# Performance work log

Measured on AMD Instinct MI355X. Metric: run time of the kernel, lower is better.

Reference implementation:

```python
import jax, jax.numpy as jnp
import numpy as np

N_LAYERS = 2
H = 16                      # num_heads
ARW = (1.0, 1.0)            # att_residual_weight
MCB = (0.0, 1.0)            # mask_clip_balancer
LN_EPS = 1e-5


def _ln(x, g, b):
    mu = jnp.mean(x, axis=-1, keepdims=True)
    var = jnp.mean(jnp.square(x - mu), axis=-1, keepdims=True)
    return (x - mu) * jax.lax.rsqrt(var + LN_EPS) * g + b


def _quick_gelu(u):
    return u * jax.nn.sigmoid(1.702 * u)


def setup_inputs() -> dict:
    key = jax.random.key(0)
    ks = jax.random.split(key, 8)
    L, B, C = 577, 8, 1024
    d_ff = 4 * C
    inp = {
        'x': jax.random.normal(ks[0], (L, B, C), jnp.float32),
        'att_bias': jax.random.normal(ks[1], (N_LAYERS, B * H, L, L), jnp.float32),
        'ln1_g': jnp.ones((N_LAYERS, C), jnp.float32),
        'ln1_b': jnp.zeros((N_LAYERS, C), jnp.float32),
        'in_w': 0.02 * jax.random.normal(ks[2], (N_LAYERS, 3 * C, C), jnp.float32),
        'in_b': jnp.zeros((N_LAYERS, 3 * C), jnp.float32),
        'out_w': 0.02 * jax.random.normal(ks[3], (N_LAYERS, C, C), jnp.float32),
        'out_b': jnp.zeros((N_LAYERS, C), jnp.float32),
        'ln2_g': jnp.ones((N_LAYERS, C), jnp.float32),
        'ln2_b': jnp.zeros((N_LAYERS, C), jnp.float32),
        'fc1_w': 0.02 * jax.random.normal(ks[4], (N_LAYERS, d_ff, C), jnp.float32),
        'fc1_b': jnp.zeros((N_LAYERS, d_ff), jnp.float32),
        'fc2_w': 0.02 * jax.random.normal(ks[5], (N_LAYERS, C, d_ff), jnp.float32),
        'fc2_b': jnp.zeros((N_LAYERS, C), jnp.float32),
    }
    return inp


def reference(x, att_bias, ln1_g, ln1_b, in_w, in_b, out_w, out_b,
              ln2_g, ln2_b, fc1_w, fc1_b, fc2_w, fc2_b):
    L, B, C = x.shape
    d = C // H
    scale = d ** -0.5  # custom_att_factor is None
    for i in range(N_LAYERS):
        # --- custom CSA attention ---
        h = _ln(x, ln1_g[i], ln1_b[i])                              # [L,B,C]
        qkv = jnp.einsum('lbc,fc->lbf', h, in_w[i]) + in_b[i]       # [L,B,3C]
        q, k, v = jnp.split(qkv, 3, axis=-1)
        to_heads = lambda t: t.reshape(L, B, H, d).transpose(1, 2, 0, 3)  # [B,H,L,d]
        q, k, v = to_heads(q), to_heads(k), to_heads(v)
        bias = att_bias[i].reshape(B, H, L, L)
        q_attn = bias + scale * jnp.einsum('bhld,bhmd->bhlm', q, q)
        k_attn = bias + scale * jnp.einsum('bhld,bhmd->bhlm', k, k)
        attn = jax.nn.softmax(q_attn, axis=-1) + jax.nn.softmax(k_attn, axis=-1)
        attn = attn * 0.5                                           # norm_att=True
        attn = jnp.mean(attn, axis=1, keepdims=True)                # avg_att=True -> [B,1,L,L]
        out = jnp.matmul(attn, v)                                   # broadcast over H -> [B,H,L,d]
        out = MCB[0] * v + MCB[1] * out
        out = out.transpose(2, 0, 1, 3).reshape(L, B, C)
        out = jnp.einsum('lbc,oc->lbo', out, out_w[i]) + out_b[i]
        x = ARW[0] * x + ARW[1] * out
        # --- MLP residual ---
        h2 = _ln(x, ln2_g[i], ln2_b[i])
        u = _quick_gelu(jnp.einsum('lbc,fc->lbf', h2, fc1_w[i]) + fc1_b[i])
        x = x + jnp.einsum('lbf,cf->lbc', u, fc2_w[i]) + fc2_b[i]
    return x
```

## Files before the change

kernel.cpp:

```cpp
#include <hip/hip_runtime.h>

typedef float f32x4 __attribute__((ext_vector_type(4)));
typedef __bf16 bf16x8 __attribute__((ext_vector_type(8)));

#define L_SEQ 577
#define BB 8
#define CC 1024
#define HH 16
#define ROWS (L_SEQ*BB)

static __device__ __forceinline__ ushort f2b(float f) {
  unsigned u = __float_as_uint(f);
  u += 0x7fffu + ((u >> 16) & 1u);
  return (ushort)(u >> 16);
}

static __device__ __forceinline__ void gld16(const void* g, void* l) {
  __builtin_amdgcn_global_load_lds((const __attribute__((address_space(1))) void*)g,
                                   (__attribute__((address_space(3))) void*)l, 16, 0, 0);
}

__global__ void cvt4_kernel(const float* __restrict__ s0, ushort* __restrict__ d0, int n0,
                            const float* __restrict__ s1, ushort* __restrict__ d1, int n1,
                            const float* __restrict__ s2, ushort* __restrict__ d2, int n2,
                            const float* __restrict__ s3, ushort* __restrict__ d3, int n3)
{
  int i = blockIdx.x * blockDim.x + threadIdx.x;
  const float* src; ushort* dst;
  if (i < n0)                { src = s0; dst = d0; }
  else if ((i -= n0) < n1)   { src = s1; dst = d1; }
  else if ((i -= n1) < n2)   { src = s2; dst = d2; }
  else if ((i -= n2) < n3)   { src = s3; dst = d3; }
  else return;
  float4 v = *(const float4*)(src + (size_t)i * 4);
  ushort4 o;
  o.x = f2b(v.x); o.y = f2b(v.y); o.z = f2b(v.z); o.w = f2b(v.w);
  *(ushort4*)(dst + (size_t)i * 4) = o;
}

template<int NP, bool DOLN>
__global__ __launch_bounds__(256)
void ln_resid_kernel(const float* __restrict__ xsrc, const float* __restrict__ parts,
                     const float* __restrict__ cbias,
                     const float* __restrict__ g, const float* __restrict__ be,
                     float* __restrict__ xdst, ushort* __restrict__ hout)
{
  const int row = blockIdx.x;
  const int t = threadIdx.x;
  float4 v = *(const float4*)(xsrc + (size_t)row * CC + t * 4);
  if (NP > 0) {
    float4 c4 = *(const float4*)(cbias + t * 4);
    v.x += c4.x; v.y += c4.y; v.z += c4.z; v.w += c4.w;
    #pragma unroll
    for (int p = 0; p < NP; ++p) {
      float4 pv = *(const float4*)(parts + ((size_t)p * ROWS + row) * CC + t * 4);
      v.x += pv.x; v.y += pv.y; v.z += pv.z; v.w += pv.w;
    }
  }
  *(float4*)(xdst + (size_t)row * CC + t * 4) = v;
  if (DOLN) {
    float s  = v.x + v.y + v.z + v.w;
    float s2 = v.x*v.x + v.y*v.y + v.z*v.z + v.w*v.w;
    #pragma unroll
    for (int sd = 1; sd < 64; sd <<= 1) { s += __shfl_xor(s, sd, 64); s2 += __shfl_xor(s2, sd, 64); }
    __shared__ float ps[4], ps2[4];
    const int w = t >> 6;
    if ((t & 63) == 0) { ps[w] = s; ps2[w] = s2; }
    __syncthreads();
    s  = ps[0] + ps[1] + ps[2] + ps[3];
    s2 = ps2[0] + ps2[1] + ps2[2] + ps2[3];
    const float mean = s * (1.f / 1024.f);
    const float var  = s2 * (1.f / 1024.f) - mean * mean;
    const float rstd = rsqrtf(var + 1e-5f);
    float4 gv = *(const float4*)(g + t * 4);
    float4 bv = *(const float4*)(be + t * 4);
    ushort4 o;
    o.x = f2b((v.x - mean) * rstd * gv.x + bv.x);
    o.y = f2b((v.y - mean) * rstd * gv.y + bv.y);
    o.z = f2b((v.z - mean) * rstd * gv.z + bv.z);
    o.w = f2b((v.w - mean) * rstd * gv.w + bv.w);
    *(ushort4*)(hout + (size_t)row * CC + t * 4) = o;
  }
}

__global__ __launch_bounds__(256)
void vt_kernel(const ushort* __restrict__ qkv, ushort* __restrict__ vt)
{
  __shared__ ushort tile[32][33];
  const int lt = blockIdx.x * 32;
  const int nt = blockIdx.y * 32;
  const int b  = blockIdx.z;
  const int tx = threadIdx.x & 31;
  const int ty = threadIdx.x >> 5;
  #pragma unroll
  for (int p = 0; p < 4; ++p) {
    int l = lt + ty + p * 8;
    ushort v = 0;
    if (l < L_SEQ) v = qkv[((size_t)l * BB + b) * 3072 + 2048 + nt + tx];
    tile[ty + p * 8][tx] = v;
  }
  __syncthreads();
  #pragma unroll
  for (int p = 0; p < 4; ++p) {
    int n = nt + ty + p * 8;
    int l = lt + tx;
    vt[((size_t)b * 1024 + n) * 608 + l] = tile[tx][ty + p * 8];
  }
}

__global__ __launch_bounds__(512, 4)
void attn_kernel(const ushort* __restrict__ qkv,
                 const float* __restrict__ bias,
                 ushort* __restrict__ attnp)
{
  __shared__ float2 red[2][2][8][16];
  const int t = threadIdx.x;
  const int lane = t & 63;
  const int w = t >> 6;
  const int fr = lane & 15;
  const int lq = lane >> 4;
  const int id = blockIdx.x;
  const int b  = id & 7;
  const int rem = id >> 3;
  const int rb = rem % 37;
  const int hg = rem / 37;
  const int r0 = rb * 16;
  const int rowl = min(r0 + fr, L_SEQ - 1);
  const size_t rbase = ((size_t)rowl * BB + b) * 3072;
  const int kc = lq * 8;

  float acc[5][4];
  #pragma unroll
  for (int it = 0; it < 5; ++it)
    #pragma unroll
    for (int r = 0; r < 4; ++r) acc[it][r] = 0.f;

  for (int h4 = 0; h4 < 4; ++h4) {
    const int h = hg * 4 + h4;
    const int qoff = h * 64;
    const int koff = CC + h * 64;
    const bf16x8 rfq0 = *(const bf16x8*)(qkv + rbase + qoff + kc);
    const bf16x8 rfq1 = *(const bf16x8*)(qkv + rbase + qoff + 32 + kc);
    const bf16x8 rfk0 = *(const bf16x8*)(qkv + rbase + koff + kc);
    const bf16x8 rfk1 = *(const bf16x8*)(qkv + rbase + koff + 32 + kc);
    const float* brow = bias + (((size_t)(b * HH + h)) * L_SEQ + rowl) * L_SEQ;
    float sq[5][4], sk[5][4];
    #pragma unroll
    for (int it = 0; it < 5; ++it) {
      const int nt = w + it * 8;
      if (nt < 37) {
        const int crow = min(nt * 16 + fr, L_SEQ - 1);
        const size_t cb = ((size_t)crow * BB + b) * 3072;
        const bf16x8 bq0 = *(const bf16x8*)(qkv + cb + qoff + kc);
        const bf16x8 bq1 = *(const bf16x8*)(qkv + cb + qoff + 32 + kc);
        const bf16x8 bk0 = *(const bf16x8*)(qkv + cb + koff + kc);
        const bf16x8 bk1 = *(const bf16x8*)(qkv + cb + koff + 32 + kc);
        const int c0 = nt * 16 + lq * 4;
        float bs[4];
        #pragma unroll
        for (int r = 0; r < 4; ++r) bs[r] = brow[min(c0 + r, L_SEQ - 1)];
        f32x4 dq = {0.f, 0.f, 0.f, 0.f};
        f32x4 dk = {0.f, 0.f, 0.f, 0.f};
        dq = __builtin_amdgcn_mfma_f32_16x16x32_bf16(bq0, rfq0, dq, 0, 0, 0);
        dq = __builtin_amdgcn_mfma_f32_16x16x32_bf16(bq1, rfq1, dq, 0, 0, 0);
        dk = __builtin_amdgcn_mfma_f32_16x16x32_bf16(bk0, rfk0, dk, 0, 0, 0);
        dk = __builtin_amdgcn_mfma_f32_16x16x32_bf16(bk1, rfk1, dk, 0, 0, 0);
        #pragma unroll
        for (int r = 0; r < 4; ++r) {
          const bool cv = (c0 + r < L_SEQ);
          sq[it][r] = cv ? (bs[r] + 0.125f * dq[r]) : -1e30f;
          sk[it][r] = cv ? (bs[r] + 0.125f * dk[r]) : -1e30f;
        }
      } else {
        #pragma unroll
        for (int r = 0; r < 4; ++r) { sq[it][r] = -1e30f; sk[it][r] = -1e30f; }
      }
    }
    float mwq = -1e30f, mwk = -1e30f;
    #pragma unroll
    for (int it = 0; it < 5; ++it)
      #pragma unroll
      for (int r = 0; r < 4; ++r) { mwq = fmaxf(mwq, sq[it][r]); mwk = fmaxf(mwk, sk[it][r]); }
    mwq = fmaxf(mwq, __shfl_xor(mwq, 16, 64)); mwq = fmaxf(mwq, __shfl_xor(mwq, 32, 64));
    mwk = fmaxf(mwk, __shfl_xor(mwk, 16, 64)); mwk = fmaxf(mwk, __shfl_xor(mwk, 32, 64));
    float swq = 0.f, swk = 0.f;
    #pragma unroll
    for (int it = 0; it < 5; ++it)
      #pragma unroll
      for (int r = 0; r < 4; ++r) {
        sq[it][r] = __expf(sq[it][r] - mwq); swq += sq[it][r];
        sk[it][r] = __expf(sk[it][r] - mwk); swk += sk[it][r];
      }
    swq += __shfl_xor(swq, 16, 64); swq += __shfl_xor(swq, 32, 64);
    swk += __shfl_xor(swk, 16, 64); swk += __shfl_xor(swk, 32, 64);
    const int p = h4 & 1;
    if (lane < 16) {
      red[p][0][w][lane] = make_float2(mwq, swq);
      red[p][1][w][lane] = make_float2(mwk, swk);
    }
    __syncthreads();
    float mq = -1e30f, mk = -1e30f;
    #pragma unroll
    for (int ww = 0; ww < 8; ++ww) {
      mq = fmaxf(mq, red[p][0][ww][fr].x);
      mk = fmaxf(mk, red[p][1][ww][fr].x);
    }
    float smq = 0.f, smk = 0.f;
    #pragma unroll
    for (int ww = 0; ww < 8; ++ww) {
      const float2 pq = red[p][0][ww][fr];
      const float2 pk = red[p][1][ww][fr];
      smq += pq.y * __expf(pq.x - mq);
      smk += pk.y * __expf(pk.x - mk);
    }
    const float fq = 0.03125f * __expf(mwq - mq) / smq;
    const float fk = 0.03125f * __expf(mwk - mk) / smk;
    #pragma unroll
    for (int it = 0; it < 5; ++it)
      #pragma unroll
      for (int r = 0; r < 4; ++r) acc[it][r] += sq[it][r] * fq + sk[it][r] * fk;
  }
  if (r0 + fr < L_SEQ) {
    ushort* dst = attnp + ((size_t)hg * 8 + b) * 608 * 608 + (size_t)(r0 + fr) * 608;
    #pragma unroll
    for (int it = 0; it < 5; ++it) {
      const int nt = w + it * 8;
      if (nt < 37) {
        ushort4 o;
        o.x = f2b(acc[it][0]); o.y = f2b(acc[it][1]);
        o.z = f2b(acc[it][2]); o.w = f2b(acc[it][3]);
        *(ushort4*)(dst + nt * 16 + lq * 4) = o;
      }
    }
  }
}

__global__ __launch_bounds__(256)
void attn_combine(const ushort* __restrict__ attnp, ushort* __restrict__ attn)
{
  const int t = threadIdx.x;
  if (t >= 152) return;
  const int l = blockIdx.x;
  const int b = blockIdx.y;
  const int c0 = t * 4;
  const size_t base = ((size_t)b * 608 + l) * 608 + c0;
  const size_t hs = (size_t)8 * 608 * 608;
  float s[4] = {0.f, 0.f, 0.f, 0.f};
  #pragma unroll
  for (int p = 0; p < 4; ++p) {
    ushort4 v = *(const ushort4*)(attnp + p * hs + base);
    s[0] += __uint_as_float((unsigned)v.x << 16);
    s[1] += __uint_as_float((unsigned)v.y << 16);
    s[2] += __uint_as_float((unsigned)v.z << 16);
    s[3] += __uint_as_float((unsigned)v.w << 16);
  }
  ushort4 o;
  const bool lv = (l < L_SEQ);
  o.x = (lv && c0 + 0 < L_SEQ) ? f2b(s[0]) : (ushort)0;
  o.y = (lv && c0 + 1 < L_SEQ) ? f2b(s[1]) : (ushort)0;
  o.z = (lv && c0 + 2 < L_SEQ) ? f2b(s[2]) : (ushort)0;
  o.w = (lv && c0 + 3 < L_SEQ) ? f2b(s[3]) : (ushort)0;
  *(ushort4*)(attn + base) = o;
}

__global__ __launch_bounds__(256, 2)
void av_gemm(const ushort* __restrict__ A, int lda, int Arows, long aStride,
             const ushort* __restrict__ B, int ldb, long bStride,
             int M, int K,
             ushort* __restrict__ outb, int ldo)
{
  __shared__ __align__(16) ushort As[128 * 32];
  __shared__ __align__(16) ushort Bs[128 * 32];
  const int t = threadIdx.x;
  const int lane = t & 63;
  const int w = t >> 6;
  const int bm = blockIdx.x, bn = blockIdx.y, bz = blockIdx.z;
  const ushort* Ab = A + (long)bz * aStride;
  const ushort* Bb = B + (long)bz * bStride;
  const int srow = t >> 2;
  const int sc = (t & 3) * 8;
  const int wr = (w >> 1) * 64;
  const int wc = (w & 1) * 64;
  const int am1 = Arows - 1;
  f32x4 acc[4][4] = {};

  const int r0a = bm * 128 + srow;
  const int r0b = bn * 128 + srow;
  for (int kt = 0; kt < K; kt += 32) {
    __syncthreads();
    gld16(Ab + (size_t)min(r0a, am1) * lda + kt + sc, (void*)(As + t * 8));
    gld16(Ab + (size_t)min(r0a + 64, am1) * lda + kt + sc, (void*)(As + 2048 + t * 8));
    gld16(Bb + (size_t)r0b * ldb + kt + sc, (void*)(Bs + t * 8));
    gld16(Bb + (size_t)(r0b + 64) * ldb + kt + sc, (void*)(Bs + 2048 + t * 8));
    asm volatile("s_waitcnt vmcnt(0)" ::: "memory");
    __syncthreads();
    bf16x8 av[4], bv[4];
    const int fr = lane & 15;
    const int kc = (lane >> 4) * 8;
    #pragma unroll
    for (int m = 0; m < 4; ++m) av[m] = *(const bf16x8*)(As + (wr + m * 16 + fr) * 32 + kc);
    #pragma unroll
    for (int n = 0; n < 4; ++n) bv[n] = *(const bf16x8*)(Bs + (wc + n * 16 + fr) * 32 + kc);
    #pragma unroll
    for (int m = 0; m < 4; ++m)
      #pragma unroll
      for (int n = 0; n < 4; ++n)
        acc[m][n] = __builtin_amdgcn_mfma_f32_16x16x32_bf16(av[m], bv[n], acc[m][n], 0, 0, 0);
  }
  const int rbase = wr + (lane >> 4) * 4;
  const int cbase = wc + (lane & 15);
  #pragma unroll
  for (int n = 0; n < 4; ++n) {
    const int gn = bn * 128 + cbase + n * 16;
    #pragma unroll
    for (int m = 0; m < 4; ++m) {
      f32x4 d = acc[m][n];
      #pragma unroll
      for (int r = 0; r < 4; ++r) {
        const int gm = bm * 128 + rbase + m * 16 + r;
        if (gm < M) outb[((size_t)gm * 8 + bz) * ldo + gn] = f2b(d[r]);
      }
    }
  }
}

#define RD_A8(BOFS, MH) \
  _Pragma("unroll") for (int ks = 0; ks < 2; ++ks) \
  _Pragma("unroll") for (int m = 0; m < 4; ++m) \
    Af[ks][m] = rdA(BOFS, MH, ks, m);

#define RD_B4(BOFS, NH) \
  _Pragma("unroll") for (int ks = 0; ks < 2; ++ks) \
  _Pragma("unroll") for (int n = 0; n < 2; ++n) \
    Bf[NH][ks][n] = rdB(BOFS, NH, ks, n);

#define MFQ(MH, NH) \
  _Pragma("unroll") for (int ks = 0; ks < 2; ++ks) \
  _Pragma("unroll") for (int m = 0; m < 4; ++m) \
  _Pragma("unroll") for (int n = 0; n < 2; ++n) \
    acc[(MH)*4+m][(NH)*2+n] = __builtin_amdgcn_mfma_f32_16x16x32_bf16( \
        Af[ks][m], Bf[NH][ks][n], acc[(MH)*4+m][(NH)*2+n], 0, 0, 0);

#define BARO() \
  __builtin_amdgcn_sched_barrier(0); \
  __builtin_amdgcn_s_barrier(); \
  asm volatile("s_waitcnt lgkmcnt(0)" ::: "memory"); \
  __builtin_amdgcn_sched_barrier(0); \
  __builtin_amdgcn_s_setprio(1);

#define MF_END() \
  __builtin_amdgcn_s_setprio(0); \
  __builtin_amdgcn_sched_barrier(0); \
  __builtin_amdgcn_s_barrier();

template<int EPI>
__global__ __launch_bounds__(512, 2)
void gemm8(const ushort* __restrict__ Ap, int lda, int Arows,
           const ushort* __restrict__ Bp, int ldb,
           int M, int Ksplit,
           const float* __restrict__ bias,
           ushort* __restrict__ outb, float* __restrict__ outf, int ldo)
{
  __shared__ __align__(16) char smem[131072];
  const int t = threadIdx.x;
  const int lane = t & 63;
  const int w = t >> 6;
  const int wm = w >> 2, wn = w & 3;
  const int gx = gridDim.x;
  const int nwg = gx * gridDim.y;
  int id = blockIdx.y * gx + blockIdx.x;
  {
    const int q8 = nwg >> 3, r8 = nwg & 7;
    const int xcd = id & 7, pos = id >> 3;
    id = (xcd < r8 ? xcd * (q8 + 1) : r8 * (q8 + 1) + (xcd - r8) * q8) + pos;
  }
  const int bm = id % gx, bn = id / gx;
  const int bz = blockIdx.z;
  const int k0 = bz * Ksplit;
  const int iters = Ksplit >> 7;
  const int fr = lane & 15, lq = lane >> 4;

  f32x4 acc[8][4] = {};
  bf16x8 Af[2][4];
  bf16x8 Bf[2][2][2];

  const int rowj0 = t >> 3,        cbj0 = t & 7;
  const int rowj1 = (t + 512) >> 3, cbj1 = (t + 512) & 7;
  const ushort* pA[2][2]; const ushort* pB[2][2];
  #pragma unroll
  for (int h = 0; h < 2; ++h) {
    pA[h][0] = Ap + (size_t)min(bm*256 + h*128 + rowj0, Arows-1) * lda + k0 + ((cbj0 ^ (rowj0 & 7)) << 3);
    pA[h][1] = Ap + (size_t)min(bm*256 + h*128 + rowj1, Arows-1) * lda + k0 + ((cbj1 ^ (rowj1 & 7)) << 3);
    pB[h][0] = Bp + (size_t)(bn*256 + h*128 + rowj0) * ldb + k0 + ((cbj0 ^ (rowj0 & 7)) << 3);
    pB[h][1] = Bp + (size_t)(bn*256 + h*128 + rowj1) * ldb + k0 + ((cbj1 ^ (rowj1 & 7)) << 3);
  }

  auto stA = [&](int kt, int bofs, int h) {
    gld16(pA[h][0] + kt * 64, smem + bofs + h * 16384 + t * 16);
    gld16(pA[h][1] + kt * 64, smem + bofs + h * 16384 + (t + 512) * 16);
  };
  auto stB = [&](int kt, int bofs, int h) {
    gld16(pB[h][0] + kt * 64, smem + bofs + 32768 + h * 16384 + t * 16);
    gld16(pB[h][1] + kt * 64, smem + bofs + 32768 + h * 16384 + (t + 512) * 16);
  };
  auto rdA = [&](int bofs, int mh, int ks, int m) -> bf16x8 {
    const int rl = wm * 64 + m * 16 + fr;
    const int cb = (ks * 4 + lq) ^ (fr & 7);
    return *(const bf16x8*)(smem + bofs + mh * 16384 + rl * 128 + cb * 16);
  };
  auto rdB = [&](int bofs, int nh, int ks, int n) -> bf16x8 {
    const int rl = wn * 32 + n * 16 + fr;
    const int cb = (ks * 4 + lq) ^ (fr & 7);
    return *(const bf16x8*)(smem + bofs + 32768 + nh * 16384 + rl * 128 + cb * 16);
  };

  stA(0, 0, 0); stB(0, 0, 0); stB(0, 0, 1); stA(0, 0, 1);
  stA(1, 65536, 0); stB(1, 65536, 1); stA(1, 65536, 1);
  asm volatile("s_waitcnt vmcnt(6)" ::: "memory");
  __builtin_amdgcn_sched_barrier(0);
  __builtin_amdgcn_s_barrier();

  for (int i = 0; i < iters; ++i) {
    const bool more = (i + 1 < iters);
    const int kt2 = 2 * i + 2;
    RD_A8(0, 0) RD_B4(0, 0)
    stB(2 * i + 1, 65536, 0);
    BARO(); MFQ(0, 0) MF_END();
    RD_B4(0, 1)
    if (more) stA(kt2, 0, 0);
    BARO(); MFQ(0, 1) MF_END();
    RD_A8(0, 1)
    if (more) stB(kt2, 0, 1);
    BARO(); MFQ(1, 1) MF_END();
    if (more) stA(kt2, 0, 1);
    BARO(); MFQ(1, 0)
    __builtin_amdgcn_s_setprio(0);
    if (more) { asm volatile("s_waitcnt vmcnt(6)" ::: "memory"); }
    else      { asm volatile("s_waitcnt vmcnt(0)" ::: "memory"); }
    __builtin_amdgcn_sched_barrier(0);
    __builtin_amdgcn_s_barrier();
    RD_A8(65536, 0) RD_B4(65536, 0)
    if (more) stB(kt2, 0, 0);
    BARO(); MFQ(0, 0) MF_END();
    RD_B4(65536, 1)
    if (more) stA(2 * i + 3, 65536, 0);
    BARO(); MFQ(0, 1) MF_END();
    RD_A8(65536, 1)
    if (more) stB(2 * i + 3, 65536, 1);
    BARO(); MFQ(1, 1) MF_END();
    if (more) stA(2 * i + 3, 65536, 1);
    BARO(); MFQ(1, 0)
    __builtin_amdgcn_s_setprio(0);
    if (more) { asm volatile("s_waitcnt vmcnt(6)" ::: "memory"); }
    __builtin_amdgcn_sched_barrier(0);
    __builtin_amdgcn_s_barrier();
  }

  #pragma unroll
  for (int mh = 0; mh < 2; ++mh)
  #pragma unroll
  for (int nh = 0; nh < 2; ++nh)
  #pragma unroll
  for (int n = 0; n < 2; ++n) {
    const int gn = bn * 256 + nh * 128 + wn * 32 + n * 16 + fr;
    const float bval = (EPI == 4) ? 0.f : bias[gn];
    #pragma unroll
    for (int m = 0; m < 4; ++m) {
      f32x4 d = acc[mh * 4 + m][nh * 2 + n];
      #pragma unroll
      for (int r = 0; r < 4; ++r) {
        const int gm = bm * 256 + mh * 128 + wm * 64 + m * 16 + lq * 4 + r;
        if (gm < M) {
          if (EPI == 0) {
            outb[(size_t)gm * ldo + gn] = f2b(d[r] + bval);
          } else if (EPI == 1) {
            float v0 = d[r] + bval;
            outb[(size_t)gm * ldo + gn] = f2b(v0 / (1.f + __expf(-1.702f * v0)));
          } else {
            outf[((size_t)bz * M + gm) * ldo + gn] = d[r];
          }
        }
      }
    }
  }
}

extern "C" void kernel_launch(void* const* d_in, const int* in_sizes, int n_in,
                              void* d_out, int out_size, void* d_ws, size_t ws_size,
                              hipStream_t stream)
{
  (void)in_sizes; (void)n_in; (void)out_size; (void)ws_size;
  const float* x_in  = (const float*)d_in[0];
  const float* attb  = (const float*)d_in[1];
  const float* ln1_g = (const float*)d_in[2];
  const float* ln1_b = (const float*)d_in[3];
  const float* in_w  = (const float*)d_in[4];
  const float* in_b  = (const float*)d_in[5];
  const float* out_w = (const float*)d_in[6];
  const float* out_b = (const float*)d_in[7];
  const float* ln2_g = (const float*)d_in[8];
  const float* ln2_b = (const float*)d_in[9];
  const float* fc1_w = (const float*)d_in[10];
  const float* fc1_b = (const float*)d_in[11];
  const float* fc2_w = (const float*)d_in[12];
  const float* fc2_b = (const float*)d_in[13];
  float* x = (float*)d_out;

  char* ws = (char*)d_ws;
  size_t off = 0;
  auto alloc = [&](size_t bytes) -> void* {
    void* p = ws + off; off += (bytes + 255) & ~(size_t)255; return p;
  };
  ushort* wIn   = (ushort*)alloc(2ull * 3072 * 1024 * 2);
  ushort* wOut  = (ushort*)alloc(2ull * 1024 * 1024 * 2);
  ushort* wF1   = (ushort*)alloc(2ull * 4096 * 1024 * 2);
  ushort* wF2   = (ushort*)alloc(2ull * 4096 * 1024 * 2);
  ushort* hbuf  = (ushort*)alloc((size_t)ROWS * 1024 * 2);
  ushort* qkv   = (ushort*)alloc((size_t)ROWS * 3072 * 2);
  ushort* vt    = (ushort*)alloc((size_t)8 * 1024 * 608 * 2);
  ushort* attn  = (ushort*)alloc((size_t)8 * 608 * 608 * 2);
  ushort* attnp = (ushort*)alloc((size_t)4 * 8 * 608 * 608 * 2);
  ushort* outlb = (ushort*)alloc((size_t)ROWS * 1024 * 2);
  float*  pbuf  = (float*)alloc((size_t)4 * ROWS * 1024 * 4);
  ushort* ubuf  = qkv;

  cvt4_kernel<<<(1572864 + 524288 + 2097152 + 2097152 + 255) / 256, 256, 0, stream>>>(
      in_w,  wIn,  1572864,
      out_w, wOut, 524288,
      fc1_w, wF1,  2097152,
      fc2_w, wF2,  2097152);
  ln_resid_kernel<0, true><<<ROWS, 256, 0, stream>>>(x_in, nullptr, nullptr,
      ln1_g, ln1_b, x, hbuf);

  for (int i = 0; i < 2; ++i) {
    gemm8<0><<<dim3(19, 12, 1), 512, 0, stream>>>(hbuf, 1024, ROWS,
        wIn + (size_t)i * 3072 * 1024, 1024,
        ROWS, 1024, in_b + i * 3072, qkv, nullptr, 3072);
    attn_kernel<<<dim3(1184, 1, 1), 512, 0, stream>>>(qkv, attb + (size_t)i * 128 * 577 * 577, attnp);
    vt_kernel<<<dim3(19, 32, 8), 256, 0, stream>>>(qkv, vt);
    attn_combine<<<dim3(608, 8), 256, 0, stream>>>(attnp, attn);
    av_gemm<<<dim3(5, 8, 8), 256, 0, stream>>>(attn, 608, 577, (long)608 * 608,
        vt, 608, (long)1024 * 608, 577, 608, outlb, 1024);
    gemm8<4><<<dim3(19, 4, 2), 512, 0, stream>>>(outlb, 1024, ROWS,
        wOut + (size_t)i * 1024 * 1024, 1024,
        ROWS, 512, nullptr, nullptr, pbuf, 1024);
    ln_resid_kernel<2, true><<<ROWS, 256, 0, stream>>>(x, pbuf, out_b + i * 1024,
        ln2_g + i * 1024, ln2_b + i * 1024, x, hbuf);
    gemm8<1><<<dim3(19, 16, 1), 512, 0, stream>>>(hbuf, 1024, ROWS,
        wF1 + (size_t)i * 4096 * 1024, 1024,
        ROWS, 1024, fc1_b + i * 4096, ubuf, nullptr, 4096);
    gemm8<4><<<dim3(19, 4, 4), 512, 0, stream>>>(ubuf, 4096, ROWS,
        wF2 + (size_t)i * 4096 * 1024, 4096,
        ROWS, 1024, nullptr, nullptr, pbuf, 1024);
    if (i == 0) {
      ln_resid_kernel<4, true><<<ROWS, 256, 0, stream>>>(x, pbuf, fc2_b,
          ln1_g + 1024, ln1_b + 1024, x, hbuf);
    } else {
      ln_resid_kernel<4, false><<<ROWS, 256, 0, stream>>>(x, pbuf, fc2_b + 1024,
          nullptr, nullptr, x, nullptr);
    }
  }
}
```

Baseline: 1.062 ms.

## Batch attention column loads per head and stage output through shared memory

The attention-score kernel now issues all bias and Q/K column-tile loads for a head up front into register arrays, then runs the MFMAs, so memory latency overlaps across the five tiles instead of being exposed one tile at a time. The output tile is written to a shared-memory buffer and stored to global memory row by row in coalesced ushort4 chunks. Occupancy hint drops from 4 to 2 blocks per CU to make room for the extra registers. Out-of-range tiles (nt>=37) are now loaded and computed with clamped addresses, which wastes a little work, and the higher register use risks lower occupancy.

```diff
diff --git a/kernel.cpp b/kernel.cpp
--- a/kernel.cpp
+++ b/kernel.cpp
@@ -108,12 +108,13 @@
   }
 }
 
-__global__ __launch_bounds__(512, 4)
+__global__ __launch_bounds__(512, 2)
 void attn_kernel(const ushort* __restrict__ qkv,
                  const float* __restrict__ bias,
                  ushort* __restrict__ attnp)
 {
   __shared__ float2 red[2][2][8][16];
+  __shared__ ushort sm[16][612];
   const int t = threadIdx.x;
   const int lane = t & 63;
   const int w = t >> 6;
@@ -129,6 +130,16 @@
   const size_t rbase = ((size_t)rowl * BB + b) * 3072;
   const int kc = lq * 8;
 
+  size_t cbs_[5];
+  int c0_[5];
+  #pragma unroll
+  for (int it = 0; it < 5; ++it) {
+    const int nt = w + it * 8;
+    const int crow = min(nt * 16 + fr, L_SEQ - 1);
+    cbs_[it] = ((size_t)crow * BB + b) * 3072;
+    c0_[it] = nt * 16 + lq * 4;
+  }
+
   float acc[5][4];
   #pragma unroll
   for (int it = 0; it < 5; ++it)
@@ -144,36 +155,36 @@
     const bf16x8 rfk0 = *(const bf16x8*)(qkv + rbase + koff + kc);
     const bf16x8 rfk1 = *(const bf16x8*)(qkv + rbase + koff + 32 + kc);
     const float* brow = bias + (((size_t)(b * HH + h)) * L_SEQ + rowl) * L_SEQ;
+
+    float bs[5][4];
+    #pragma unroll
+    for (int it = 0; it < 5; ++it)
+      #pragma unroll
+      for (int r = 0; r < 4; ++r) bs[it][r] = brow[min(c0_[it] + r, L_SEQ - 1)];
+    bf16x8 cq0[5], cq1[5], ck0[5], ck1[5];
+    #pragma unroll
+    for (int it = 0; it < 5; ++it) {
+      const ushort* cp = qkv + cbs_[it];
+      cq0[it] = *(const bf16x8*)(cp + qoff + kc);
+      cq1[it] = *(const bf16x8*)(cp + qoff + 32 + kc);
+      ck0[it] = *(const bf16x8*)(cp + koff + kc);
+      ck1[it] = *(const bf16x8*)(cp + koff + 32 + kc);
+    }
+
     float sq[5][4], sk[5][4];
     #pragma unroll
     for (int it = 0; it < 5; ++it) {
-      const int nt = w + it * 8;
-      if (nt < 37) {
-        const int crow = min(nt * 16 + fr, L_SEQ - 1);
-        const size_t cb = ((size_t)crow * BB + b) * 3072;
-        const bf16x8 bq0 = *(const bf16x8*)(qkv + cb + qoff + kc);
-        const bf16x8 bq1 = *(const bf16x8*)(qkv + cb + qoff + 32 + kc);
-        const bf16x8 bk0 = *(const bf16x8*)(qkv + cb + koff + kc);
-        const bf16x8 bk1 = *(const bf16x8*)(qkv + cb + koff + 32 + kc);
-        const int c0 = nt * 16 + lq * 4;
-        float bs[4];
-        #pragma unroll
-        for (int r = 0; r < 4; ++r) bs[r] = brow[min(c0 + r, L_SEQ - 1)];
-        f32x4 dq = {0.f, 0.f, 0.f, 0.f};
-        f32x4 dk = {0.f, 0.f, 0.f, 0.f};
-        dq = __builtin_amdgcn_mfma_f32_16x16x32_bf16(bq0, rfq0, dq, 0, 0, 0);
-        dq = __builtin_amdgcn_mfma_f32_16x16x32_bf16(bq1, rfq1, dq, 0, 0, 0);
-        dk = __builtin_amdgcn_mfma_f32_16x16x32_bf16(bk0, rfk0, dk, 0, 0, 0);
-        dk = __builtin_amdgcn_mfma_f32_16x16x32_bf16(bk1, rfk1, dk, 0, 0, 0);
-        #pragma unroll
-        for (int r = 0; r < 4; ++r) {
-          const bool cv = (c0 + r < L_SEQ);
-          sq[it][r] = cv ? (bs[r] + 0.125f * dq[r]) : -1e30f;
-          sk[it][r] = cv ? (bs[r] + 0.125f * dk[r]) : -1e30f;
-        }
-      } else {
-        #pragma unroll
-        for (int r = 0; r < 4; ++r) { sq[it][r] = -1e30f; sk[it][r] = -1e30f; }
+      f32x4 dq = {0.f, 0.f, 0.f, 0.f};
+      f32x4 dk = {0.f, 0.f, 0.f, 0.f};
+      dq = __builtin_amdgcn_mfma_f32_16x16x32_bf16(cq0[it], rfq0, dq, 0, 0, 0);
+      dq = __builtin_amdgcn_mfma_f32_16x16x32_bf16(cq1[it], rfq1, dq, 0, 0, 0);
+      dk = __builtin_amdgcn_mfma_f32_16x16x32_bf16(ck0[it], rfk0, dk, 0, 0, 0);
+      dk = __builtin_amdgcn_mfma_f32_16x16x32_bf16(ck1[it], rfk1, dk, 0, 0, 0);
+      #pragma unroll
+      for (int r = 0; r < 4; ++r) {
+        const bool cv = (c0_[it] + r < L_SEQ);
+        sq[it][r] = cv ? (bs[it][r] + 0.125f * dq[r]) : -1e30f;
+        sk[it][r] = cv ? (bs[it][r] + 0.125f * dk[r]) : -1e30f;
       }
     }
     float mwq = -1e30f, mwk = -1e30f;
@@ -220,18 +231,23 @@
       #pragma unroll
       for (int r = 0; r < 4; ++r) acc[it][r] += sq[it][r] * fq + sk[it][r] * fk;
   }
-  if (r0 + fr < L_SEQ) {
-    ushort* dst = attnp + ((size_t)hg * 8 + b) * 608 * 608 + (size_t)(r0 + fr) * 608;
-    #pragma unroll
-    for (int it = 0; it < 5; ++it) {
-      const int nt = w + it * 8;
-      if (nt < 37) {
-        ushort4 o;
-        o.x = f2b(acc[it][0]); o.y = f2b(acc[it][1]);
-        o.z = f2b(acc[it][2]); o.w = f2b(acc[it][3]);
-        *(ushort4*)(dst + nt * 16 + lq * 4) = o;
-      }
-    }
+
+  #pragma unroll
+  for (int it = 0; it < 5; ++it) {
+    if (c0_[it] < 608) {
+      ushort4 o;
+      o.x = f2b(acc[it][0]); o.y = f2b(acc[it][1]);
+      o.z = f2b(acc[it][2]); o.w = f2b(acc[it][3]);
+      *(ushort4*)&sm[fr][c0_[it]] = o;
+    }
+  }
+  __syncthreads();
+  ushort* dst = attnp + ((size_t)hg * 8 + b) * 608 * 608 + (size_t)r0 * 608;
+  for (int j = t; j < 16 * 152; j += 512) {
+    const int row = j / 152;
+    const int c4 = (j % 152) * 4;
+    if (r0 + row < L_SEQ)
+      *(ushort4*)(dst + (size_t)row * 608 + c4) = *(const ushort4*)&sm[row][c4];
   }
 }
 
```

Result: faster. 1.022 ms (-3.8%).
